# Kernel tuning notes

Measured on AMD Instinct MI355X. Metric: run time of the kernel, lower is better.

Reference implementation:

```python
import jax, jax.numpy as jnp
import numpy as np

B, S, D, H = 1, 2048, 1024, 16
HD = D // H
FF = 4 * D
EPS_LN = 1e-5
EPS_ATTN = 1e-6


def _layernorm(x, g, b):
    mu = jnp.mean(x, axis=-1, keepdims=True)
    var = jnp.mean(jnp.square(x - mu), axis=-1, keepdims=True)
    return (x - mu) * jax.lax.rsqrt(var + EPS_LN) * g + b


def setup_inputs() -> dict:
    key = jax.random.key(0)
    ks = jax.random.split(key, 12)
    w = lambda k, shape: (jax.random.normal(k, shape, jnp.float32) * 0.02)
    return {
        "x": jax.random.normal(ks[0], (B, S, D), jnp.float32),
        "Wq": w(ks[1], (D, D)), "bq": jnp.zeros((D,), jnp.float32),
        "Wk": w(ks[2], (D, D)), "bk": jnp.zeros((D,), jnp.float32),
        "Wv": w(ks[3], (D, D)), "bv": jnp.zeros((D,), jnp.float32),
        "Wo": w(ks[4], (D, D)), "bo": jnp.zeros((D,), jnp.float32),
        "W1": w(ks[5], (FF, D)), "bb1": jnp.zeros((FF,), jnp.float32),
        "W2": w(ks[6], (D, FF)), "bb2": jnp.zeros((D,), jnp.float32),
        "g1": jnp.ones((D,), jnp.float32), "be1": jnp.zeros((D,), jnp.float32),
        "g2": jnp.ones((D,), jnp.float32), "be2": jnp.zeros((D,), jnp.float32),
    }


def reference(x, Wq, bq, Wk, bk, Wv, bv, Wo, bo, W1, bb1, W2, bb2, g1, be1, g2, be2):
    # --- pre-norm causal linear attention ---
    h = _layernorm(x, g1, be1)                     # (B,S,D)
    def heads(t):
        return t.reshape(B, S, H, HD).transpose(0, 2, 1, 3)  # (B,H,S,hd)
    q = heads(h @ Wq.T + bq)
    k = heads(h @ Wk.T + bk)
    v = heads(h @ Wv.T + bv)
    # feature map phi(x) = elu(x) + 1 (strictly positive)
    q = jax.nn.elu(q) + 1.0
    k = jax.nn.elu(k) + 1.0
    # causal cumulative state: S_t = sum_{i<=t} k_i v_i^T ; z_t = sum_{i<=t} k_i
    kv = jnp.cumsum(jnp.einsum("bhsd,bhse->bhsde", k, v), axis=2)  # (B,H,S,hd,hd)
    z = jnp.cumsum(k, axis=2)                                       # (B,H,S,hd)
    num = jnp.einsum("bhsd,bhsde->bhse", q, kv)                    # (B,H,S,hd)
    den = jnp.einsum("bhsd,bhsd->bhs", q, z) + EPS_ATTN
    attn = (num / den[..., None]).transpose(0, 2, 1, 3).reshape(B, S, D)
    attn = attn @ Wo.T + bo
    x = x + attn
    # --- FFN (GELU exact, matching torch nn.GELU default) ---
    h2 = _layernorm(x, g2, be2)
    ff = jax.nn.gelu(h2 @ W1.T + bb1, approximate=False) @ W2.T + bb2
    return x + ff
```

## Files before the change

kernel.cpp:

```cpp
#include <hip/hip_runtime.h>
#include <hip/hip_bf16.h>
#include <math.h>

constexpr int S  = 2048;
constexpr int D  = 1024;
constexpr int H  = 16;
constexpr int HD = 64;
constexpr int FF = 4096;
constexpr int NC  = 32;
constexpr int CHK = 64;
constexpr int QS  = 3 * D;

typedef __attribute__((ext_vector_type(8))) short bf16x8;
typedef __attribute__((ext_vector_type(4))) float f32x4;
typedef __attribute__((ext_vector_type(16))) float f32x16;

__device__ inline unsigned short f2bf(float f) {
    unsigned int u = __float_as_uint(f);
    u = (u + 0x7FFFu + ((u >> 16) & 1u)) >> 16;
    return (unsigned short)u;
}

constexpr int DD4 = D * D / 4;
constexpr int FD4 = FF * D / 4;
constexpr int CVT_TOTAL4 = 4 * DD4 + 2 * FD4;

__global__ __launch_bounds__(256) void cvt6(const float* __restrict__ Wq,
                                            const float* __restrict__ Wk,
                                            const float* __restrict__ Wv,
                                            const float* __restrict__ Wo,
                                            const float* __restrict__ W1,
                                            const float* __restrict__ W2,
                                            unsigned short* __restrict__ Wqkvb,
                                            unsigned short* __restrict__ Wob,
                                            unsigned short* __restrict__ W1b,
                                            unsigned short* __restrict__ W2b) {
    int i = blockIdx.x * 256 + threadIdx.x;
    if (i >= CVT_TOTAL4) return;
    const float* s;
    unsigned short* dp;
    if (i < DD4)                 { s = Wq + (size_t)i * 4;               dp = Wqkvb + (size_t)i * 4; }
    else if (i < 2 * DD4)        { s = Wk + (size_t)(i - DD4) * 4;       dp = Wqkvb + (size_t)i * 4; }
    else if (i < 3 * DD4)        { s = Wv + (size_t)(i - 2 * DD4) * 4;   dp = Wqkvb + (size_t)i * 4; }
    else if (i < 4 * DD4)        { s = Wo + (size_t)(i - 3 * DD4) * 4;   dp = Wob + (size_t)(i - 3 * DD4) * 4; }
    else if (i < 4 * DD4 + FD4)  { s = W1 + (size_t)(i - 4 * DD4) * 4;   dp = W1b + (size_t)(i - 4 * DD4) * 4; }
    else                         { s = W2 + (size_t)(i - 4 * DD4 - FD4) * 4; dp = W2b + (size_t)(i - 4 * DD4 - FD4) * 4; }
    float4 v = *(const float4*)s;
    ushort4 o = { f2bf(v.x), f2bf(v.y), f2bf(v.z), f2bf(v.w) };
    *(ushort4*)dp = o;
}

__global__ __launch_bounds__(256) void layernorm_bf16(const float* __restrict__ x,
                                                      const float* __restrict__ g,
                                                      const float* __restrict__ b,
                                                      unsigned short* __restrict__ out) {
    const int row = blockIdx.x, tid = threadIdx.x;
    float4 v = ((const float4*)(x + (size_t)row * D))[tid];
    float s  = v.x + v.y + v.z + v.w;
    float ss = v.x*v.x + v.y*v.y + v.z*v.z + v.w*v.w;
    #pragma unroll
    for (int off = 32; off > 0; off >>= 1) {
        s  += __shfl_down(s, off);
        ss += __shfl_down(ss, off);
    }
    __shared__ float sw[4], ssw[4];
    if ((tid & 63) == 0) { sw[tid >> 6] = s; ssw[tid >> 6] = ss; }
    __syncthreads();
    s  = sw[0] + sw[1] + sw[2] + sw[3];
    ss = ssw[0] + ssw[1] + ssw[2] + ssw[3];
    const float mu = s * (1.0f / D);
    const float rs = rsqrtf(ss * (1.0f / D) - mu * mu + 1e-5f);
    float4 gv = ((const float4*)g)[tid];
    float4 bv = ((const float4*)b)[tid];
    ushort4 o = { f2bf((v.x - mu) * rs * gv.x + bv.x),
                  f2bf((v.y - mu) * rs * gv.y + bv.y),
                  f2bf((v.z - mu) * rs * gv.z + bv.z),
                  f2bf((v.w - mu) * rs * gv.w + bv.w) };
    ((ushort4*)(out + (size_t)row * D))[tid] = o;
}

template <int KS>
__global__ __launch_bounds__(256) void reduce_ln(const float* __restrict__ part,
                                                 const float* __restrict__ bias,
                                                 const float* __restrict__ res,
                                                 float* __restrict__ x2,
                                                 const float* __restrict__ g,
                                                 const float* __restrict__ b,
                                                 unsigned short* __restrict__ out) {
    const int row = blockIdx.x, tid = threadIdx.x;
    const size_t i4 = (size_t)row * 256 + tid;
    float4 a = ((const float4*)part)[i4];
    #pragma unroll
    for (int z = 1; z < KS; ++z) {
        float4 p = ((const float4*)part)[(size_t)z * S * 256 + i4];
        a.x += p.x; a.y += p.y; a.z += p.z; a.w += p.w;
    }
    float4 bi = ((const float4*)bias)[tid];
    float4 r  = ((const float4*)res)[i4];
    a.x += bi.x + r.x; a.y += bi.y + r.y; a.z += bi.z + r.z; a.w += bi.w + r.w;
    ((float4*)x2)[i4] = a;
    float s  = a.x + a.y + a.z + a.w;
    float ss = a.x*a.x + a.y*a.y + a.z*a.z + a.w*a.w;
    #pragma unroll
    for (int off = 32; off > 0; off >>= 1) {
        s  += __shfl_down(s, off);
        ss += __shfl_down(ss, off);
    }
    __shared__ float sw[4], ssw[4];
    if ((tid & 63) == 0) { sw[tid >> 6] = s; ssw[tid >> 6] = ss; }
    __syncthreads();
    s  = sw[0] + sw[1] + sw[2] + sw[3];
    ss = ssw[0] + ssw[1] + ssw[2] + ssw[3];
    const float mu = s * (1.0f / D);
    const float rs = rsqrtf(ss * (1.0f / D) - mu * mu + 1e-5f);
    float4 gv = ((const float4*)g)[tid];
    float4 bv = ((const float4*)b)[tid];
    ushort4 o = { f2bf((a.x - mu) * rs * gv.x + bv.x),
                  f2bf((a.y - mu) * rs * gv.y + bv.y),
                  f2bf((a.z - mu) * rs * gv.z + bv.z),
                  f2bf((a.w - mu) * rs * gv.w + bv.w) };
    ((ushort4*)(out + (size_t)row * D))[tid] = o;
}

template <int KS>
__global__ __launch_bounds__(256) void reduce_bias_res(const float* __restrict__ part,
                                                       const float* __restrict__ bias,
                                                       const float* __restrict__ res,
                                                       float* __restrict__ out,
                                                       int N4, int total4) {
    int i = blockIdx.x * 256 + threadIdx.x;
    if (i >= total4) return;
    float4 a = ((const float4*)part)[i];
    #pragma unroll
    for (int z = 1; z < KS; ++z) {
        float4 p = ((const float4*)part)[(size_t)z * total4 + i];
        a.x += p.x; a.y += p.y; a.z += p.z; a.w += p.w;
    }
    float4 b = ((const float4*)bias)[i % N4];
    float4 r = ((const float4*)res)[i];
    a.x += b.x + r.x; a.y += b.y + r.y; a.z += b.z + r.z; a.w += b.w + r.w;
    ((float4*)out)[i] = a;
}

enum { EPI_F32 = 0, EPI_QKV = 1, EPI_GELU_BF16 = 2, EPI_PART = 3 };

template <int EPI>
__global__ __launch_bounds__(512, 2) void gemm_bt2(const unsigned short* __restrict__ A,
                                                   const unsigned short* __restrict__ W,
                                                   const float* __restrict__ bias,
                                                   const float* __restrict__ bias2,
                                                   const float* __restrict__ bias3,
                                                   void* __restrict__ outp,
                                                   int M, int N, int K, int kSplit) {
    __shared__ unsigned short As[3][256 * 64];
    __shared__ unsigned short Bs[3][128 * 64];
    const int tid   = threadIdx.x;
    const int tileM = blockIdx.x * 256;
    const int tileN = blockIdx.y * 128;
    const int w    = tid >> 6, lane = tid & 63;
    const int wm   = (w >> 1) * 64, wn = (w & 1) * 64;
    const int l31  = lane & 31, lhi = lane >> 5;
    const int sw32 = (l31 >> 1) & 7;
    const int kLen   = K / kSplit;
    const int kStart = blockIdx.z * kLen;
    const int nt     = kLen >> 6;

    f32x16 acc[2][2];
    #pragma unroll
    for (int i = 0; i < 2; ++i)
        #pragma unroll
        for (int j = 0; j < 2; ++j) acc[i][j] = (f32x16)(0.0f);

    auto stage = [&](int buf, int k0) {
        #pragma unroll
        for (int p = 0; p < 4; ++p) {
            const int c   = p * 512 + tid;
            const int row = c >> 3;
            const int kc  = (c & 7) ^ ((row >> 1) & 7);
            __builtin_amdgcn_global_load_lds(
                (const __attribute__((address_space(1))) unsigned int*)
                    (A + (size_t)(tileM + row) * K + k0 + kc * 8),
                (__attribute__((address_space(3))) unsigned int*)&As[buf][c * 8],
                16, 0, 0);
        }
        #pragma unroll
        for (int p = 0; p < 2; ++p) {
            const int c   = p * 512 + tid;
            const int row = c >> 3;
            const int kc  = (c & 7) ^ ((row >> 1) & 7);
            __builtin_amdgcn_global_load_lds(
                (const __attribute__((address_space(1))) unsigned int*)
                    (W + (size_t)(tileN + row) * K + k0 + kc * 8),
                (__attribute__((address_space(3))) unsigned int*)&Bs[buf][c * 8],
                16, 0, 0);
        }
    };

    stage(0, kStart);
    if (nt > 1) stage(1, kStart + 64);

    int k0 = kStart;
    for (int t = 0; t < nt; ++t, k0 += 64) {
        if (t + 1 < nt) asm volatile("s_waitcnt vmcnt(6) lgkmcnt(0)" ::: "memory");
        else            asm volatile("s_waitcnt vmcnt(0) lgkmcnt(0)" ::: "memory");
        __builtin_amdgcn_s_barrier();
        if (t + 2 < nt) stage((t + 2) % 3, k0 + 128);

        const unsigned short* Ab = &As[t % 3][0];
        const unsigned short* Bb = &Bs[t % 3][0];
        bf16x8 af[4][2], bfv[4][2];
        #pragma unroll
        for (int s = 0; s < 4; ++s) {
            const int slot = (2 * s + lhi) ^ sw32;
            #pragma unroll
            for (int i = 0; i < 2; ++i)
                af[s][i] = *(const bf16x8*)&Ab[(wm + i * 32 + l31) * 64 + slot * 8];
            #pragma unroll
            for (int j = 0; j < 2; ++j)
                bfv[s][j] = *(const bf16x8*)&Bb[(wn + j * 32 + l31) * 64 + slot * 8];
        }
        __builtin_amdgcn_s_setprio(1);
        #pragma unroll
        for (int s = 0; s < 4; ++s)
            #pragma unroll
            for (int i = 0; i < 2; ++i)
                #pragma unroll
                for (int j = 0; j < 2; ++j)
                    acc[i][j] = __builtin_amdgcn_mfma_f32_32x32x16_bf16(af[s][i], bfv[s][j], acc[i][j], 0, 0, 0);
        __builtin_amdgcn_s_setprio(0);
    }

    #pragma unroll
    for (int i = 0; i < 2; ++i) {
        #pragma unroll
        for (int j = 0; j < 2; ++j) {
            const int col = tileN + wn + j * 32 + l31;
            #pragma unroll
            for (int q = 0; q < 4; ++q) {
                const int rbase = tileM + wm + i * 32 + q * 8 + lhi * 4;
                #pragma unroll
                for (int r = 0; r < 4; ++r) {
                    const int row = rbase + r;
                    const size_t off = (size_t)row * N + col;
                    float v = acc[i][j][q * 4 + r];
                    if constexpr (EPI == EPI_PART) {
                        ((float*)outp)[(size_t)blockIdx.z * (size_t)M * (size_t)N + off] = v;
                    } else if constexpr (EPI == EPI_QKV) {
                        float bc = (col < D) ? bias[col] : ((col < 2 * D) ? bias2[col - D] : bias3[col - 2 * D]);
                        v += bc;
                        if (col < 2 * D) v = v > 0.0f ? v + 1.0f : __expf(v);
                        ((float*)outp)[off] = v;
                    } else if constexpr (EPI == EPI_GELU_BF16) {
                        v += bias[col];
                        float gl = 0.5f * v * (1.0f + erff(v * 0.70710678118654752f));
                        ((unsigned short*)outp)[off] = f2bf(gl);
                    } else {
                        v += bias[col];
                        ((float*)outp)[off] = v;
                    }
                }
            }
        }
    }
}

__global__ __launch_bounds__(256) void attn_chunk_sums(const float* __restrict__ qkv,
                                                       float* __restrict__ KVc,
                                                       float* __restrict__ Zc) {
    const int c = blockIdx.x, h = blockIdx.y, tid = threadIdx.x;
    __shared__ float Kc[CHK * HD], Vc[CHK * HD];
    const int s0 = c * CHK;
    #pragma unroll
    for (int p = 0; p < 4; ++p) {
        int cc = p * 256 + tid;
        int t = cc >> 4, dp = (cc & 15) * 4;
        *(float4*)&Kc[t * HD + dp] = *(const float4*)(qkv + (size_t)(s0 + t) * QS + D     + h * HD + dp);
        *(float4*)&Vc[t * HD + dp] = *(const float4*)(qkv + (size_t)(s0 + t) * QS + 2 * D + h * HD + dp);
    }
    __syncthreads();
    const int d = tid >> 2, e0 = (tid & 3) * 16;
    float acc[16];
    #pragma unroll
    for (int j = 0; j < 16; ++j) acc[j] = 0.0f;
    float zacc = 0.0f;
    for (int t = 0; t < CHK; ++t) {
        float kv = Kc[t * HD + d];
        zacc += kv;
        #pragma unroll
        for (int j = 0; j < 16; ++j) acc[j] += kv * Vc[t * HD + e0 + j];
    }
    float* op = KVc + ((size_t)(h * NC + c) * HD + d) * HD + e0;
    #pragma unroll
    for (int j = 0; j < 16; ++j) op[j] = acc[j];
    if ((tid & 3) == 0) Zc[(size_t)(h * NC + c) * HD + d] = zacc;
}

__global__ __launch_bounds__(256) void attn_prefix(float* __restrict__ KVc,
                                                   float* __restrict__ Zc) {
    const int h = blockIdx.y;
    const int elem = blockIdx.x * 256 + threadIdx.x;
    size_t base = (size_t)h * NC * (HD * HD) + elem;
    float v[NC];
    #pragma unroll
    for (int c = 0; c < NC; ++c) v[c] = KVc[base + (size_t)c * (HD * HD)];
    float run = 0.0f;
    #pragma unroll
    for (int c = 0; c < NC; ++c) { float t = v[c]; v[c] = run; run += t; }
    #pragma unroll
    for (int c = 0; c < NC; ++c) KVc[base + (size_t)c * (HD * HD)] = v[c];
    if (blockIdx.x == 0 && threadIdx.x < HD) {
        size_t zb = (size_t)h * NC * HD + threadIdx.x;
        float z[NC];
        #pragma unroll
        for (int c = 0; c < NC; ++c) z[c] = Zc[zb + (size_t)c * HD];
        float zr = 0.0f;
        #pragma unroll
        for (int c = 0; c < NC; ++c) { float t = z[c]; z[c] = zr; zr += t; }
        #pragma unroll
        for (int c = 0; c < NC; ++c) Zc[zb + (size_t)c * HD] = z[c];
    }
}

__global__ __launch_bounds__(256) void attn_out(const float* __restrict__ qkv,
                                                const float* __restrict__ KVpre,
                                                const float* __restrict__ Zpre,
                                                unsigned short* __restrict__ attn) {
    const int c = blockIdx.x, h = blockIdx.y, tid = threadIdx.x;
    __shared__ float Qc[CHK * HD], KVs[CHK * HD], Pre[HD * HD], Sc[CHK * CHK];
    __shared__ float zp[HD], den[CHK];
    const int s0 = c * CHK;
    #pragma unroll
    for (int p = 0; p < 4; ++p) {
        int cc = p * 256 + tid;
        int t = cc >> 4, dp = (cc & 15) * 4;
        *(float4*)&Qc[t * HD + dp]  = *(const float4*)(qkv + (size_t)(s0 + t) * QS +     h * HD + dp);
        *(float4*)&KVs[t * HD + dp] = *(const float4*)(qkv + (size_t)(s0 + t) * QS + D + h * HD + dp);
        ((float4*)Pre)[cc] = *(const float4*)(KVpre + (size_t)(h * NC + c) * (HD * HD) + cc * 4);
    }
    if (tid < HD) zp[tid] = Zpre[(size_t)(h * NC + c) * HD + tid];
    __syncthreads();

    const int tt = tid >> 2, i0 = (tid & 3) * 16;
    for (int i = i0; i < i0 + 16; ++i) {
        float sv = 0.0f;
        for (int d2 = 0; d2 < HD; ++d2) sv += Qc[tt * HD + d2] * KVs[i * HD + d2];
        Sc[tt * CHK + i] = (i <= tt) ? sv : 0.0f;
    }
    __syncthreads();

    if (tid < CHK) {
        float dv = 1e-6f;
        for (int d2 = 0; d2 < HD; ++d2) dv += Qc[tid * HD + d2] * zp[d2];
        for (int i = 0; i < CHK; ++i) dv += Sc[tid * CHK + i];
        den[tid] = dv;
    }
    #pragma unroll
    for (int p = 0; p < 4; ++p) {
        int cc = p * 256 + tid;
        int t = cc >> 4, dp = (cc & 15) * 4;
        *(float4*)&KVs[t * HD + dp] = *(const float4*)(qkv + (size_t)(s0 + t) * QS + 2 * D + h * HD + dp);
    }
    __syncthreads();

    float o[16];
    #pragma unroll
    for (int j = 0; j < 16; ++j) o[j] = 0.0f;
    for (int d2 = 0; d2 < HD; ++d2) {
        float qv = Qc[tt * HD + d2];
        float sv = Sc[tt * CHK + d2];
        #pragma unroll
        for (int j = 0; j < 16; ++j)
            o[j] += qv * Pre[d2 * HD + i0 + j] + sv * KVs[d2 * HD + i0 + j];
    }
    const float inv = 1.0f / den[tt];
    unsigned short* op = attn + (size_t)(s0 + tt) * D + h * HD + i0;
    #pragma unroll
    for (int j0 = 0; j0 < 16; j0 += 4) {
        ushort4 ov = { f2bf(o[j0] * inv), f2bf(o[j0 + 1] * inv),
                       f2bf(o[j0 + 2] * inv), f2bf(o[j0 + 3] * inv) };
        *(ushort4*)(op + j0) = ov;
    }
}

extern "C" void kernel_launch(void* const* d_in, const int* in_sizes, int n_in,
                              void* d_out, int out_size, void* d_ws, size_t ws_size,
                              hipStream_t stream) {
    const float* x   = (const float*)d_in[0];
    const float* Wq  = (const float*)d_in[1];
    const float* bq  = (const float*)d_in[2];
    const float* Wk  = (const float*)d_in[3];
    const float* bk  = (const float*)d_in[4];
    const float* Wv  = (const float*)d_in[5];
    const float* bv  = (const float*)d_in[6];
    const float* Wo  = (const float*)d_in[7];
    const float* bo  = (const float*)d_in[8];
    const float* W1  = (const float*)d_in[9];
    const float* b1  = (const float*)d_in[10];
    const float* W2  = (const float*)d_in[11];
    const float* b2  = (const float*)d_in[12];
    const float* g1  = (const float*)d_in[13];
    const float* be1 = (const float*)d_in[14];
    const float* g2  = (const float*)d_in[15];
    const float* be2 = (const float*)d_in[16];
    float* out = (float*)d_out;

    char* wsp = (char*)d_ws;
    auto alloc = [&](size_t bytes) {
        char* p = wsp;
        wsp += (bytes + 255) & ~(size_t)255;
        return p;
    };
    unsigned short* h1   = (unsigned short*)alloc((size_t)S * D * 2);
    unsigned short* attn = (unsigned short*)alloc((size_t)S * D * 2);
    unsigned short* gbuf = (unsigned short*)alloc((size_t)S * FF * 2);
    float* x2   = (float*)alloc((size_t)S * D * 4);
    unsigned short* Wqkvb = (unsigned short*)alloc((size_t)3 * D * D * 2);
    unsigned short* Wob   = (unsigned short*)alloc((size_t)D * D * 2);
    unsigned short* W1b   = (unsigned short*)alloc((size_t)FF * D * 2);
    unsigned short* W2b   = (unsigned short*)alloc((size_t)D * FF * 2);
    float* KVc  = (float*)alloc((size_t)H * NC * HD * HD * 4);
    float* Zc   = (float*)alloc((size_t)H * NC * HD * 4);
    char* uni = (char*)alloc((size_t)32 * 1024 * 1024);
    float* qkv   = (float*)uni;
    float* parts = (float*)uni;

    cvt6<<<(CVT_TOTAL4 + 255) / 256, 256, 0, stream>>>(Wq, Wk, Wv, Wo, W1, W2,
                                                       Wqkvb, Wob, W1b, W2b);

    layernorm_bf16<<<S, 256, 0, stream>>>(x, g1, be1, h1);

    gemm_bt2<EPI_QKV><<<dim3(S / 256, 3 * D / 128, 1), 512, 0, stream>>>(
        h1, Wqkvb, bq, bk, bv, qkv, S, 3 * D, D, 1);

    attn_chunk_sums<<<dim3(NC, H), 256, 0, stream>>>(qkv, KVc, Zc);
    attn_prefix<<<dim3(16, H), 256, 0, stream>>>(KVc, Zc);
    attn_out<<<dim3(NC, H), 256, 0, stream>>>(qkv, KVc, Zc, attn);

    gemm_bt2<EPI_PART><<<dim3(S / 256, D / 128, 4), 512, 0, stream>>>(
        attn, Wob, nullptr, nullptr, nullptr, parts, S, D, D, 4);
    reduce_ln<4><<<S, 256, 0, stream>>>(parts, bo, x, x2, g2, be2, h1);

    gemm_bt2<EPI_GELU_BF16><<<dim3(S / 256, FF / 128, 1), 512, 0, stream>>>(
        h1, W1b, b1, nullptr, nullptr, gbuf, S, FF, D, 1);

    gemm_bt2<EPI_PART><<<dim3(S / 256, D / 128, 4), 512, 0, stream>>>(
        gbuf, W2b, nullptr, nullptr, nullptr, parts, S, D, FF, 4);
    reduce_bias_res<4><<<(S * D / 4 + 255) / 256, 256, 0, stream>>>(
        parts, b2, x2, out, D / 4, S * D / 4);
}
```

Baseline: 291.0 us.

## Replace split-K GEMMs with smaller-tile GEMM and fuse bias/residual epilogue

Removes split-K from the two N=1024 GEMMs (Wo and W2) and adds a new 128x64 tile GEMM kernel. That kernel launches 256 blocks without partial-sum buffers. The W2 GEMM now adds bias and residual in its epilogue, so the separate reduce_bias_res kernel is gone. The Wo GEMM still writes a single partial that reduce_ln<1> consumes. Weight conversion and the first layernorm are merged into one launch. This drops partial-buffer traffic and kernel launches, at the cost of a long serial K loop (K=4096) per block with less parallelism.

After: 308.9 us. 6.2% more time.

```diff
diff --git a/kernel.cpp b/kernel.cpp
--- a/kernel.cpp
+++ b/kernel.cpp
@@ -24,37 +24,39 @@
 constexpr int DD4 = D * D / 4;
 constexpr int FD4 = FF * D / 4;
 constexpr int CVT_TOTAL4 = 4 * DD4 + 2 * FD4;
-
-__global__ __launch_bounds__(256) void cvt6(const float* __restrict__ Wq,
-                                            const float* __restrict__ Wk,
-                                            const float* __restrict__ Wv,
-                                            const float* __restrict__ Wo,
-                                            const float* __restrict__ W1,
-                                            const float* __restrict__ W2,
-                                            unsigned short* __restrict__ Wqkvb,
-                                            unsigned short* __restrict__ Wob,
-                                            unsigned short* __restrict__ W1b,
-                                            unsigned short* __restrict__ W2b) {
-    int i = blockIdx.x * 256 + threadIdx.x;
-    if (i >= CVT_TOTAL4) return;
-    const float* s;
-    unsigned short* dp;
-    if (i < DD4)                 { s = Wq + (size_t)i * 4;               dp = Wqkvb + (size_t)i * 4; }
-    else if (i < 2 * DD4)        { s = Wk + (size_t)(i - DD4) * 4;       dp = Wqkvb + (size_t)i * 4; }
-    else if (i < 3 * DD4)        { s = Wv + (size_t)(i - 2 * DD4) * 4;   dp = Wqkvb + (size_t)i * 4; }
-    else if (i < 4 * DD4)        { s = Wo + (size_t)(i - 3 * DD4) * 4;   dp = Wob + (size_t)(i - 3 * DD4) * 4; }
-    else if (i < 4 * DD4 + FD4)  { s = W1 + (size_t)(i - 4 * DD4) * 4;   dp = W1b + (size_t)(i - 4 * DD4) * 4; }
-    else                         { s = W2 + (size_t)(i - 4 * DD4 - FD4) * 4; dp = W2b + (size_t)(i - 4 * DD4 - FD4) * 4; }
-    float4 v = *(const float4*)s;
-    ushort4 o = { f2bf(v.x), f2bf(v.y), f2bf(v.z), f2bf(v.w) };
-    *(ushort4*)dp = o;
-}
-
-__global__ __launch_bounds__(256) void layernorm_bf16(const float* __restrict__ x,
-                                                      const float* __restrict__ g,
-                                                      const float* __restrict__ b,
-                                                      unsigned short* __restrict__ out) {
-    const int row = blockIdx.x, tid = threadIdx.x;
+constexpr int CVT_BLOCKS = CVT_TOTAL4 / 256;
+
+__global__ __launch_bounds__(256) void cvt_ln(const float* __restrict__ x,
+                                              const float* __restrict__ g,
+                                              const float* __restrict__ b,
+                                              unsigned short* __restrict__ lnout,
+                                              const float* __restrict__ Wq,
+                                              const float* __restrict__ Wk,
+                                              const float* __restrict__ Wv,
+                                              const float* __restrict__ Wo,
+                                              const float* __restrict__ W1,
+                                              const float* __restrict__ W2,
+                                              unsigned short* __restrict__ Wqkvb,
+                                              unsigned short* __restrict__ Wob,
+                                              unsigned short* __restrict__ W1b,
+                                              unsigned short* __restrict__ W2b) {
+    const int tid = threadIdx.x;
+    if (blockIdx.x >= S) {
+        int i = (blockIdx.x - S) * 256 + tid;
+        const float* s;
+        unsigned short* dp;
+        if (i < DD4)                 { s = Wq + (size_t)i * 4;               dp = Wqkvb + (size_t)i * 4; }
+        else if (i < 2 * DD4)        { s = Wk + (size_t)(i - DD4) * 4;       dp = Wqkvb + (size_t)i * 4; }
+        else if (i < 3 * DD4)        { s = Wv + (size_t)(i - 2 * DD4) * 4;   dp = Wqkvb + (size_t)i * 4; }
+        else if (i < 4 * DD4)        { s = Wo + (size_t)(i - 3 * DD4) * 4;   dp = Wob + (size_t)(i - 3 * DD4) * 4; }
+        else if (i < 4 * DD4 + FD4)  { s = W1 + (size_t)(i - 4 * DD4) * 4;   dp = W1b + (size_t)(i - 4 * DD4) * 4; }
+        else                         { s = W2 + (size_t)(i - 4 * DD4 - FD4) * 4; dp = W2b + (size_t)(i - 4 * DD4 - FD4) * 4; }
+        float4 v = *(const float4*)s;
+        ushort4 o = { f2bf(v.x), f2bf(v.y), f2bf(v.z), f2bf(v.w) };
+        *(ushort4*)dp = o;
+        return;
+    }
+    const int row = blockIdx.x;
     float4 v = ((const float4*)(x + (size_t)row * D))[tid];
     float s  = v.x + v.y + v.z + v.w;
     float ss = v.x*v.x + v.y*v.y + v.z*v.z + v.w*v.w;
@@ -76,7 +78,7 @@
                   f2bf((v.y - mu) * rs * gv.y + bv.y),
                   f2bf((v.z - mu) * rs * gv.z + bv.z),
                   f2bf((v.w - mu) * rs * gv.w + bv.w) };
-    ((ushort4*)(out + (size_t)row * D))[tid] = o;
+    ((ushort4*)(lnout + (size_t)row * D))[tid] = o;
 }
 
 template <int KS>
@@ -122,27 +124,7 @@
     ((ushort4*)(out + (size_t)row * D))[tid] = o;
 }
 
-template <int KS>
-__global__ __launch_bounds__(256) void reduce_bias_res(const float* __restrict__ part,
-                                                       const float* __restrict__ bias,
-                                                       const float* __restrict__ res,
-                                                       float* __restrict__ out,
-                                                       int N4, int total4) {
-    int i = blockIdx.x * 256 + threadIdx.x;
-    if (i >= total4) return;
-    float4 a = ((const float4*)part)[i];
-    #pragma unroll
-    for (int z = 1; z < KS; ++z) {
-        float4 p = ((const float4*)part)[(size_t)z * total4 + i];
-        a.x += p.x; a.y += p.y; a.z += p.z; a.w += p.w;
-    }
-    float4 b = ((const float4*)bias)[i % N4];
-    float4 r = ((const float4*)res)[i];
-    a.x += b.x + r.x; a.y += b.y + r.y; a.z += b.z + r.z; a.w += b.w + r.w;
-    ((float4*)out)[i] = a;
-}
-
-enum { EPI_F32 = 0, EPI_QKV = 1, EPI_GELU_BF16 = 2, EPI_PART = 3 };
+enum { EPI_F32 = 0, EPI_QKV = 1, EPI_GELU_BF16 = 2, EPI_PART = 3, EPI_BIAS_RES = 4 };
 
 template <int EPI>
 __global__ __launch_bounds__(512, 2) void gemm_bt2(const unsigned short* __restrict__ A,
@@ -151,7 +133,7 @@
                                                    const float* __restrict__ bias2,
                                                    const float* __restrict__ bias3,
                                                    void* __restrict__ outp,
-                                                   int M, int N, int K, int kSplit) {
+                                                   int M, int N, int K) {
     __shared__ unsigned short As[3][256 * 64];
     __shared__ unsigned short Bs[3][128 * 64];
     const int tid   = threadIdx.x;
@@ -161,9 +143,7 @@
     const int wm   = (w >> 1) * 64, wn = (w & 1) * 64;
     const int l31  = lane & 31, lhi = lane >> 5;
     const int sw32 = (l31 >> 1) & 7;
-    const int kLen   = K / kSplit;
-    const int kStart = blockIdx.z * kLen;
-    const int nt     = kLen >> 6;
+    const int nt   = K >> 6;
 
     f32x16 acc[2][2];
     #pragma unroll
@@ -196,10 +176,10 @@
         }
     };
 
-    stage(0, kStart);
-    if (nt > 1) stage(1, kStart + 64);
-
-    int k0 = kStart;
+    stage(0, 0);
+    if (nt > 1) stage(1, 64);
+
+    int k0 = 0;
     for (int t = 0; t < nt; ++t, k0 += 64) {
         if (t + 1 < nt) asm volatile("s_waitcnt vmcnt(6) lgkmcnt(0)" ::: "memory");
         else            asm volatile("s_waitcnt vmcnt(0) lgkmcnt(0)" ::: "memory");
@@ -243,9 +223,7 @@
                     const int row = rbase + r;
                     const size_t off = (size_t)row * N + col;
                     float v = acc[i][j][q * 4 + r];
-                    if constexpr (EPI == EPI_PART) {
-                        ((float*)outp)[(size_t)blockIdx.z * (size_t)M * (size_t)N + off] = v;
-                    } else if constexpr (EPI == EPI_QKV) {
+                    if constexpr (EPI == EPI_QKV) {
                         float bc = (col < D) ? bias[col] : ((col < 2 * D) ? bias2[col - D] : bias3[col - 2 * D]);
                         v += bc;
                         if (col < 2 * D) v = v > 0.0f ? v + 1.0f : __expf(v);
@@ -258,6 +236,105 @@
                         v += bias[col];
                         ((float*)outp)[off] = v;
                     }
+                }
+            }
+        }
+    }
+}
+
+template <int EPI>
+__global__ __launch_bounds__(256, 2) void gemm_n64(const unsigned short* __restrict__ A,
+                                                   const unsigned short* __restrict__ W,
+                                                   const float* __restrict__ bias,
+                                                   const float* __restrict__ res,
+                                                   void* __restrict__ outp,
+                                                   int M, int N, int K) {
+    __shared__ unsigned short As[3][128 * 64];
+    __shared__ unsigned short Bs[3][64 * 64];
+    const int tid   = threadIdx.x;
+    const int tileM = blockIdx.x * 128;
+    const int tileN = blockIdx.y * 64;
+    const int w    = tid >> 6, lane = tid & 63;
+    const int wm   = (w >> 1) * 64, wn = (w & 1) * 32;
+    const int l31  = lane & 31, lhi = lane >> 5;
+    const int sw32 = (l31 >> 1) & 7;
+    const int nt   = K >> 6;
+
+    f32x16 acc[2];
+    #pragma unroll
+    for (int i = 0; i < 2; ++i) acc[i] = (f32x16)(0.0f);
+
+    auto stage = [&](int buf, int k0) {
+        #pragma unroll
+        for (int p = 0; p < 4; ++p) {
+            const int c   = p * 256 + tid;
+            const int row = c >> 3;
+            const int kc  = (c & 7) ^ ((row >> 1) & 7);
+            __builtin_amdgcn_global_load_lds(
+                (const __attribute__((address_space(1))) unsigned int*)
+                    (A + (size_t)(tileM + row) * K + k0 + kc * 8),
+                (__attribute__((address_space(3))) unsigned int*)&As[buf][c * 8],
+                16, 0, 0);
+        }
+        #pragma unroll
+        for (int p = 0; p < 2; ++p) {
+            const int c   = p * 256 + tid;
+            const int row = c >> 3;
+            const int kc  = (c & 7) ^ ((row >> 1) & 7);
+            __builtin_amdgcn_global_load_lds(
+                (const __attribute__((address_space(1))) unsigned int*)
+                    (W + (size_t)(tileN + row) * K + k0 + kc * 8),
+                (__attribute__((address_space(3))) unsigned int*)&Bs[buf][c * 8],
+                16, 0, 0);
+        }
+    };
+
+    stage(0, 0);
+    if (nt > 1) stage(1, 64);
+
+    int k0 = 0;
+    for (int t = 0; t < nt; ++t, k0 += 64) {
+        if (t + 1 < nt) asm volatile("s_waitcnt vmcnt(6) lgkmcnt(0)" ::: "memory");
+        else            asm volatile("s_waitcnt vmcnt(0) lgkmcnt(0)" ::: "memory");
+        __builtin_amdgcn_s_barrier();
+        if (t + 2 < nt) stage((t + 2) % 3, k0 + 128);
+
+        const unsigned short* Ab = &As[t % 3][0];
+        const unsigned short* Bb = &Bs[t % 3][0];
+        bf16x8 af[4][2], bfv[4];
+        #pragma unroll
+        for (int s = 0; s < 4; ++s) {
+            const int slot = (2 * s + lhi) ^ sw32;
+            #pragma unroll
+            for (int i = 0; i < 2; ++i)
+                af[s][i] = *(const bf16x8*)&Ab[(wm + i * 32 + l31) * 64 + slot * 8];
+            bfv[s] = *(const bf16x8*)&Bb[(wn + l31) * 64 + slot * 8];
+        }
+        __builtin_amdgcn_s_setprio(1);
+        #pragma unroll
+        for (int s = 0; s < 4; ++s)
+            #pragma unroll
+            for (int i = 0; i < 2; ++i)
+                acc[i] = __builtin_amdgcn_mfma_f32_32x32x16_bf16(af[s][i], bfv[s], acc[i], 0, 0, 0);
+        __builtin_amdgcn_s_setprio(0);
+    }
+
+    #pragma unroll
+    for (int i = 0; i < 2; ++i) {
+        const int col = tileN + wn + l31;
+        #pragma unroll
+        for (int q = 0; q < 4; ++q) {
+            const int rbase = tileM + wm + i * 32 + q * 8 + lhi * 4;
+            #pragma unroll
+            for (int r = 0; r < 4; ++r) {
+                const int row = rbase + r;
+                const size_t off = (size_t)row * N + col;
+                float v = acc[i][q * 4 + r];
+                if constexpr (EPI == EPI_BIAS_RES) {
+                    v += bias[col] + res[off];
+                    ((float*)outp)[off] = v;
+                } else {
+                    ((float*)outp)[off] = v;
                 }
             }
         }
@@ -424,27 +501,24 @@
     float* qkv   = (float*)uni;
     float* parts = (float*)uni;
 
-    cvt6<<<(CVT_TOTAL4 + 255) / 256, 256, 0, stream>>>(Wq, Wk, Wv, Wo, W1, W2,
-                                                       Wqkvb, Wob, W1b, W2b);
-
-    layernorm_bf16<<<S, 256, 0, stream>>>(x, g1, be1, h1);
+    cvt_ln<<<S + CVT_BLOCKS, 256, 0, stream>>>(x, g1, be1, h1,
+                                               Wq, Wk, Wv, Wo, W1, W2,
+                                               Wqkvb, Wob, W1b, W2b);
 
     gemm_bt2<EPI_QKV><<<dim3(S / 256, 3 * D / 128, 1), 512, 0, stream>>>(
-        h1, Wqkvb, bq, bk, bv, qkv, S, 3 * D, D, 1);
+        h1, Wqkvb, bq, bk, bv, qkv, S, 3 * D, D);
 
     attn_chunk_sums<<<dim3(NC, H), 256, 0, stream>>>(qkv, KVc, Zc);
     attn_prefix<<<dim3(16, H), 256, 0, stream>>>(KVc, Zc);
     attn_out<<<dim3(NC, H), 256, 0, stream>>>(qkv, KVc, Zc, attn);
 
-    gemm_bt2<EPI_PART><<<dim3(S / 256, D / 128, 4), 512, 0, stream>>>(
-        attn, Wob, nullptr, nullptr, nullptr, parts, S, D, D, 4);
-    reduce_ln<4><<<S, 256, 0, stream>>>(parts, bo, x, x2, g2, be2, h1);
+    gemm_n64<EPI_PART><<<dim3(S / 128, D / 64, 1), 256, 0, stream>>>(
+        attn, Wob, nullptr, nullptr, parts, S, D, D);
+    reduce_ln<1><<<S, 256, 0, stream>>>(parts, bo, x, x2, g2, be2, h1);
 
     gemm_bt2<EPI_GELU_BF16><<<dim3(S / 256, FF / 128, 1), 512, 0, stream>>>(
-        h1, W1b, b1, nullptr, nullptr, gbuf, S, FF, D, 1);
-
-    gemm_bt2<EPI_PART><<<dim3(S / 256, D / 128, 4), 512, 0, stream>>>(
-        gbuf, W2b, nullptr, nullptr, nullptr, parts, S, D, FF, 4);
-    reduce_bias_res<4><<<(S * D / 4 + 255) / 256, 256, 0, stream>>>(
-        parts, b2, x2, out, D / 4, S * D / 4);
-}
+        h1, W1b, b1, nullptr, nullptr, gbuf, S, FF, D);
+
+    gemm_n64<EPI_BIAS_RES><<<dim3(S / 128, D / 64, 1), 256, 0, stream>>>(
+        gbuf, W2b, b2, x2, out, S, D, FF);
+}
```
